# Optimization experiments

Hardware: AMD Instinct MI355X
Metric: run time of the kernel (lower is better)

The kernel has to match this reference:

```python
import jax, jax.numpy as jnp
import numpy as np

B, P, L = 256, 16, 4
NUM_ENTITY, NUM_NODE = 500000, 512
E, C1, C2 = 128, 512, 256


def setup_inputs() -> dict:
    key = jax.random.key(0)
    ks = jax.random.split(key, 13)
    inp = {
        "start_ids": jax.random.randint(ks[0], (B, P), 0, NUM_ENTITY, dtype=jnp.int32),
        "end_ids": jax.random.randint(ks[1], (B, P), 0, NUM_ENTITY, dtype=jnp.int32),
        "module_ids": jax.random.randint(ks[2], (B, P, L), 0, NUM_NODE, dtype=jnp.int32),
        "counts": jax.random.randint(ks[3], (B, P), 1, 10, dtype=jnp.int32),
        # learned parameters
        "embed": jax.random.normal(ks[4], (NUM_ENTITY, E), dtype=jnp.float32) * 0.02,
        "W": jax.random.normal(ks[5], (NUM_NODE, E, E), dtype=jnp.float32) * (1.0 / np.sqrt(E)),
        "b": jax.random.normal(ks[6], (NUM_NODE, E), dtype=jnp.float32) * 0.01,
        "W1": jax.random.normal(ks[7], (C1, 2 * E), dtype=jnp.float32) * (1.0 / np.sqrt(2 * E)),
        "b1": jnp.zeros((C1,), jnp.float32),
        "W2": jax.random.normal(ks[8], (C2, C1), dtype=jnp.float32) * (1.0 / np.sqrt(C1)),
        "b2": jnp.zeros((C2,), jnp.float32),
        "W3": jax.random.normal(ks[9], (1, C2), dtype=jnp.float32) * (1.0 / np.sqrt(C2)),
        "b3": jnp.zeros((1,), jnp.float32),
    }
    return inp


def reference(start_ids, end_ids, module_ids, counts, embed, W, b, W1, b1, W2, b2, W3, b3):
    # Embed path endpoints: [B, P, E]
    x = embed[start_ids]
    y = embed[end_ids]

    # Apply the same per-node Linear chain to both endpoint embeddings.
    # Scan over the L path steps; gather the step's weight matrices per path.
    def step(carry, mids):  # mids: [B, P]
        x, y = carry
        Wg = W[mids]            # [B, P, E, E] (out, in)
        bg = b[mids]            # [B, P, E]
        x = jnp.einsum('bpi,bpoi->bpo', x, Wg) + bg
        y = jnp.einsum('bpi,bpoi->bpo', y, Wg) + bg
        return (x, y), None

    (x, y), _ = jax.lax.scan(step, (x, y), jnp.transpose(module_ids, (2, 0, 1)))

    feat = jnp.concatenate([x, y], axis=-1)          # [B, P, 2E]
    c = counts.astype(feat.dtype)                    # path multiplicities
    pooled = jnp.einsum('bp,bpf->bf', c, feat) / jnp.sum(c, axis=1, keepdims=True)

    h = jax.nn.relu(pooled @ W1.T + b1)
    h = jax.nn.relu(h @ W2.T + b2)
    out = jax.nn.sigmoid(h @ W3.T + b3)              # [B, 1]
    return out
```

## Files before the change

kernel.cpp:

```cpp
#include <hip/hip_runtime.h>
#include <math.h>

#define BB 256
#define PP 16
#define LL 4
#define EE 128
#define NPATH (BB*PP)
#define NMOD 512
#define CC1 512
#define CC2 256

#define WS_STATE   0
#define WS_CNT     (NPATH*2*EE*4)
#define WS_OFF     (WS_CNT  + LL*NMOD*4)
#define WS_LISTS   (WS_OFF  + LL*NMOD*4)
#define WS_END     (WS_LISTS + LL*NPATH*4)

#define FMA4(A, S, Wv) do{ (A).x=fmaf((S),(Wv).x,(A).x); (A).y=fmaf((S),(Wv).y,(A).y); \
                           (A).z=fmaf((S),(Wv).z,(A).z); (A).w=fmaf((S),(Wv).w,(A).w);}while(0)

__device__ __forceinline__ unsigned short f2bf(float f) {
    unsigned u = __float_as_uint(f);
    u = (u + 0x7fffu + ((u >> 16) & 1u)) >> 16;
    return (unsigned short)u;
}
__device__ __forceinline__ float bf2f(unsigned short s) {
    return __uint_as_float(((unsigned)s) << 16);
}

__global__ __launch_bounds__(512) void k_bucket(
    const int* __restrict__ module_ids, int* __restrict__ cnt_g,
    int* __restrict__ off_g, int* __restrict__ lists)
{
    const int l = blockIdx.x, t = threadIdx.x;
    __shared__ int s[NMOD];
    __shared__ int pos[NMOD];
    s[t] = 0;
    __syncthreads();
    int mloc[8];
    #pragma unroll
    for (int j = 0; j < 8; ++j) {
        const int bp = j*512 + t;
        const int m = module_ids[bp*LL + l];
        mloc[j] = m;
        atomicAdd(&s[m], 1);
    }
    __syncthreads();
    const int c = s[t];
    for (int d = 1; d < NMOD; d <<= 1) {
        const int v = (t >= d) ? s[t-d] : 0;
        __syncthreads();
        s[t] += v;
        __syncthreads();
    }
    const int excl = s[t] - c;
    cnt_g[l*NMOD + t] = c;
    off_g[l*NMOD + t] = excl;
    pos[t] = excl;
    __syncthreads();
    #pragma unroll
    for (int j = 0; j < 8; ++j) {
        const int p = atomicAdd(&pos[mloc[j]], 1);
        lists[l*NPATH + p] = j*512 + t;
    }
}

__global__ __launch_bounds__(256) void k_seed(
    const int* __restrict__ start_ids, const int* __restrict__ end_ids,
    const float* __restrict__ embed, float* __restrict__ state)
{
    const int bp = blockIdx.x, t = threadIdx.x;
    const int id = (t < EE) ? start_ids[bp] : end_ids[bp];
    state[(size_t)bp*256 + t] = embed[(size_t)id*EE + (t & (EE-1))];
}

__global__ __launch_bounds__(256) void k_step(
    const int l, const float* __restrict__ W, const float* __restrict__ bvec,
    const int* __restrict__ cnt, const int* __restrict__ off,
    const int* __restrict__ lists, float* __restrict__ state)
{
    __shared__ unsigned short Ws[128*128];
    __shared__ float vb[32*128];
    const int m = blockIdx.x, t = threadIdx.x;
    const int n = cnt[l*NMOD + m];
    if (n == 0) return;

    {
        const int oc = t & 127, kh = t >> 7;
        const float4* Wr = (const float4*)(W + ((size_t)m*128 + oc)*128 + kh*64);
        #pragma unroll
        for (int it = 0; it < 16; ++it) {
            const float4 wv = Wr[it];
            const int k0 = kh*64 + it*4;
            Ws[(k0+0)*128 + oc] = f2bf(wv.x);
            Ws[(k0+1)*128 + oc] = f2bf(wv.y);
            Ws[(k0+2)*128 + oc] = f2bf(wv.z);
            Ws[(k0+3)*128 + oc] = f2bf(wv.w);
        }
    }

    const int* lst = lists + l*NPATH + off[l*NMOD + m];
    const int nr = 2*n;
    const int cg = t & 31;
    const int rg = t >> 5;
    const float4 bias4 = ((const float4*)(bvec + (size_t)m*128))[cg];

    for (int base = 0; base < nr; base += 32) {
        __syncthreads();
        #pragma unroll
        for (int it = 0; it < 4; ++it) {
            const int flat = it*256 + t;
            const int row = flat >> 5, c4 = flat & 31;
            float4 v = make_float4(0.f, 0.f, 0.f, 0.f);
            const int r = base + row;
            if (r < nr) {
                const int pv = lst[r >> 1]*2 + (r & 1);
                v = ((const float4*)state)[pv*32 + c4];
            }
            ((float4*)vb)[row*32 + c4] = v;
        }
        __syncthreads();

        float4 acc0 = make_float4(0,0,0,0), acc1 = make_float4(0,0,0,0);
        float4 acc2 = make_float4(0,0,0,0), acc3 = make_float4(0,0,0,0);
        const int r0 = rg*4;
        #pragma unroll 4
        for (int k0 = 0; k0 < 128; k0 += 4) {
            const ushort4 u0 = *(const ushort4*)&Ws[(k0+0)*128 + 4*cg];
            const ushort4 u1 = *(const ushort4*)&Ws[(k0+1)*128 + 4*cg];
            const ushort4 u2 = *(const ushort4*)&Ws[(k0+2)*128 + 4*cg];
            const ushort4 u3 = *(const ushort4*)&Ws[(k0+3)*128 + 4*cg];
            const int q = k0 >> 2;
            const float4 va0 = ((const float4*)vb)[(r0+0)*32 + q];
            const float4 va1 = ((const float4*)vb)[(r0+1)*32 + q];
            const float4 va2 = ((const float4*)vb)[(r0+2)*32 + q];
            const float4 va3 = ((const float4*)vb)[(r0+3)*32 + q];
            const float4 w0 = make_float4(bf2f(u0.x), bf2f(u0.y), bf2f(u0.z), bf2f(u0.w));
            const float4 w1 = make_float4(bf2f(u1.x), bf2f(u1.y), bf2f(u1.z), bf2f(u1.w));
            const float4 w2 = make_float4(bf2f(u2.x), bf2f(u2.y), bf2f(u2.z), bf2f(u2.w));
            const float4 w3 = make_float4(bf2f(u3.x), bf2f(u3.y), bf2f(u3.z), bf2f(u3.w));
            FMA4(acc0, va0.x, w0); FMA4(acc0, va0.y, w1); FMA4(acc0, va0.z, w2); FMA4(acc0, va0.w, w3);
            FMA4(acc1, va1.x, w0); FMA4(acc1, va1.y, w1); FMA4(acc1, va1.z, w2); FMA4(acc1, va1.w, w3);
            FMA4(acc2, va2.x, w0); FMA4(acc2, va2.y, w1); FMA4(acc2, va2.z, w2); FMA4(acc2, va2.w, w3);
            FMA4(acc3, va3.x, w0); FMA4(acc3, va3.y, w1); FMA4(acc3, va3.z, w2); FMA4(acc3, va3.w, w3);
        }
        float4 accs[4] = {acc0, acc1, acc2, acc3};
        #pragma unroll
        for (int i = 0; i < 4; ++i) {
            const int r = base + r0 + i;
            if (r < nr) {
                const int pv = lst[r >> 1]*2 + (r & 1);
                float4 o = make_float4(accs[i].x + bias4.x, accs[i].y + bias4.y,
                                       accs[i].z + bias4.z, accs[i].w + bias4.w);
                ((float4*)state)[pv*32 + cg] = o;
            }
        }
    }
}

__global__ __launch_bounds__(256) void k_mlp(
    const int* __restrict__ counts, const float* __restrict__ state,
    const float* __restrict__ W1, const float* __restrict__ b1,
    const float* __restrict__ W2, const float* __restrict__ b2,
    const float* __restrict__ W3, const float* __restrict__ b3,
    float* __restrict__ out)
{
    const int t = threadIdx.x;
    const int b0 = blockIdx.x * 2;
    __shared__ float pl[2][256];
    __shared__ float h1s[2][CC1];
    __shared__ float h2s[2][CC2];
    __shared__ float red[256];

    #pragma unroll
    for (int r = 0; r < 2; ++r) {
        const int b = b0 + r;
        float acc = 0.f, cs = 0.f;
        #pragma unroll
        for (int p = 0; p < PP; ++p) {
            const float cc = (float)counts[b*PP + p];
            cs += cc;
            acc = fmaf(cc, state[((size_t)(b*PP + p))*256 + t], acc);
        }
        pl[r][t] = acc / cs;
    }
    __syncthreads();

    #pragma unroll
    for (int hh = 0; hh < 2; ++hh) {
        const int col = t + hh*256;
        const float4* w4 = (const float4*)(W1 + (size_t)col*256);
        float a0 = b1[col], a1 = a0;
        for (int q = 0; q < 64; ++q) {
            const float4 wv = w4[q];
            const float4 v0 = ((const float4*)pl[0])[q];
            const float4 v1 = ((const float4*)pl[1])[q];
            a0 = fmaf(wv.x,v0.x, fmaf(wv.y,v0.y, fmaf(wv.z,v0.z, fmaf(wv.w,v0.w, a0))));
            a1 = fmaf(wv.x,v1.x, fmaf(wv.y,v1.y, fmaf(wv.z,v1.z, fmaf(wv.w,v1.w, a1))));
        }
        h1s[0][col] = fmaxf(a0, 0.f);
        h1s[1][col] = fmaxf(a1, 0.f);
    }
    __syncthreads();

    {
        const float4* w4 = (const float4*)(W2 + (size_t)t*512);
        float a0 = b2[t], a1 = a0;
        for (int q = 0; q < 128; ++q) {
            const float4 wv = w4[q];
            const float4 v0 = ((const float4*)h1s[0])[q];
            const float4 v1 = ((const float4*)h1s[1])[q];
            a0 = fmaf(wv.x,v0.x, fmaf(wv.y,v0.y, fmaf(wv.z,v0.z, fmaf(wv.w,v0.w, a0))));
            a1 = fmaf(wv.x,v1.x, fmaf(wv.y,v1.y, fmaf(wv.z,v1.z, fmaf(wv.w,v1.w, a1))));
        }
        h2s[0][t] = fmaxf(a0, 0.f);
        h2s[1][t] = fmaxf(a1, 0.f);
    }
    __syncthreads();

    {
        const int r = t >> 7, k = t & 127;
        red[t] = fmaf(W3[k], h2s[r][k], W3[k+128] * h2s[r][k+128]);
        for (int s = 64; s > 0; s >>= 1) {
            __syncthreads();
            if ((t & 127) < s) red[t] += red[t + s];
        }
        __syncthreads();
        if ((t & 127) == 0)
            out[b0 + r] = 1.f / (1.f + expf(-(red[t] + b3[0])));
    }
}

__global__ __launch_bounds__(256) void fb_path_kernel(
    const int* __restrict__ start_ids, const int* __restrict__ end_ids,
    const int* __restrict__ module_ids,
    const float* __restrict__ embed, const float* __restrict__ W,
    const float* __restrict__ bvec, float* __restrict__ feat_ws)
{
    const int bp = blockIdx.x, t = threadIdx.x;
    __shared__ float bufx[2][EE];
    __shared__ float bufy[2][EE];
    const int sid = start_ids[bp], eid = end_ids[bp];
    if (t < EE) bufx[0][t]      = embed[(size_t)sid*EE + t];
    else        bufy[0][t - EE] = embed[(size_t)eid*EE + (t - EE)];
    __syncthreads();
    const int o = t & (EE - 1);
    int cur = 0;
    for (int l = 0; l < LL; ++l) {
        const int mid = module_ids[bp*LL + l];
        const float*  vin  = (t < EE) ? bufx[cur] : bufy[cur];
        const float4* v4   = (const float4*)vin;
        const float4* wrow = (const float4*)(W + ((size_t)mid*EE + o)*EE);
        float acc = bvec[(size_t)mid*EE + o];
        #pragma unroll 8
        for (int k = 0; k < EE/4; ++k) {
            const float4 wv = wrow[k]; const float4 v = v4[k];
            acc = fmaf(wv.x,v.x, fmaf(wv.y,v.y, fmaf(wv.z,v.z, fmaf(wv.w,v.w, acc))));
        }
        if (t < EE) bufx[1-cur][o] = acc; else bufy[1-cur][o] = acc;
        __syncthreads();
        cur = 1 - cur;
    }
    feat_ws[(size_t)bp*(2*EE) + t] = (t < EE) ? bufx[cur][t] : bufy[cur][t - EE];
}

__global__ __launch_bounds__(256) void fb_mlp_kernel(
    const int* __restrict__ counts, const float* __restrict__ feat_ws,
    const float* __restrict__ W1, const float* __restrict__ b1,
    const float* __restrict__ W2, const float* __restrict__ b2,
    const float* __restrict__ W3, const float* __restrict__ b3,
    float* __restrict__ out)
{
    const int t = threadIdx.x, b0 = blockIdx.x*8;
    __shared__ float pooled[8][2*EE];
    __shared__ float h1s[8][CC1];
    __shared__ float h2s[8][CC2];
    for (int j = 0; j < 8; ++j) {
        const int b = b0 + j;
        float acc = 0.f, csum = 0.f;
        #pragma unroll
        for (int p = 0; p < PP; ++p) {
            const float cc = (float)counts[b*PP + p];
            csum += cc;
            acc = fmaf(cc, feat_ws[(size_t)(b*PP + p)*(2*EE) + t], acc);
        }
        pooled[j][t] = acc / csum;
    }
    __syncthreads();
    for (int rh = 0; rh < 2; ++rh) {
        const int r = t + rh*256;
        float acc[8]; const float bb = b1[r];
        #pragma unroll
        for (int j = 0; j < 8; ++j) acc[j] = bb;
        const float4* w4 = (const float4*)(W1 + (size_t)r*(2*EE));
        for (int k = 0; k < (2*EE)/4; ++k) {
            const float4 wv = w4[k];
            #pragma unroll
            for (int j = 0; j < 8; ++j) {
                const float4 v = ((const float4*)pooled[j])[k];
                acc[j] = fmaf(wv.x,v.x, fmaf(wv.y,v.y, fmaf(wv.z,v.z, fmaf(wv.w,v.w, acc[j]))));
            }
        }
        #pragma unroll
        for (int j = 0; j < 8; ++j) h1s[j][r] = fmaxf(acc[j], 0.f);
    }
    __syncthreads();
    {
        const int r = t;
        float acc[8]; const float bb = b2[r];
        #pragma unroll
        for (int j = 0; j < 8; ++j) acc[j] = bb;
        const float4* w4 = (const float4*)(W2 + (size_t)r*CC1);
        for (int k = 0; k < CC1/4; ++k) {
            const float4 wv = w4[k];
            #pragma unroll
            for (int j = 0; j < 8; ++j) {
                const float4 v = ((const float4*)h1s[j])[k];
                acc[j] = fmaf(wv.x,v.x, fmaf(wv.y,v.y, fmaf(wv.z,v.z, fmaf(wv.w,v.w, acc[j]))));
            }
        }
        #pragma unroll
        for (int j = 0; j < 8; ++j) h2s[j][r] = fmaxf(acc[j], 0.f);
    }
    __syncthreads();
    const int j = t >> 5, k = t & 31;
    float partial = 0.f;
    #pragma unroll
    for (int m = 0; m < CC2; m += 32)
        partial = fmaf(W3[k + m], h2s[j][k + m], partial);
    #pragma unroll
    for (int s = 16; s >= 1; s >>= 1) partial += __shfl_down(partial, s, 32);
    if (k == 0) out[b0 + j] = 1.f / (1.f + expf(-(partial + b3[0])));
}

extern "C" void kernel_launch(void* const* d_in, const int* in_sizes, int n_in,
                              void* d_out, int out_size, void* d_ws, size_t ws_size,
                              hipStream_t stream)
{
    const int*   start_ids  = (const int*)d_in[0];
    const int*   end_ids    = (const int*)d_in[1];
    const int*   module_ids = (const int*)d_in[2];
    const int*   counts     = (const int*)d_in[3];
    const float* embed      = (const float*)d_in[4];
    const float* W          = (const float*)d_in[5];
    const float* bvec       = (const float*)d_in[6];
    const float* W1         = (const float*)d_in[7];
    const float* b1         = (const float*)d_in[8];
    const float* W2         = (const float*)d_in[9];
    const float* b2         = (const float*)d_in[10];
    const float* W3         = (const float*)d_in[11];
    const float* b3         = (const float*)d_in[12];
    float* out = (float*)d_out;
    char*  ws  = (char*)d_ws;

    if (ws_size >= (size_t)WS_END) {
        float* state = (float*)(ws + WS_STATE);
        int*   cnt   = (int*)(ws + WS_CNT);
        int*   offs  = (int*)(ws + WS_OFF);
        int*   lists = (int*)(ws + WS_LISTS);

        k_bucket<<<LL, 512, 0, stream>>>(module_ids, cnt, offs, lists);
        k_seed<<<NPATH, 256, 0, stream>>>(start_ids, end_ids, embed, state);
        for (int l = 0; l < LL; ++l)
            k_step<<<NMOD, 256, 0, stream>>>(l, W, bvec, cnt, offs, lists, state);
        k_mlp<<<BB/2, 256, 0, stream>>>(counts, state, W1, b1, W2, b2, W3, b3, out);
    } else {
        float* feat_ws = (float*)d_ws;
        fb_path_kernel<<<NPATH, 256, 0, stream>>>(start_ids, end_ids, module_ids,
                                                  embed, W, bvec, feat_ws);
        fb_mlp_kernel<<<BB/8, 256, 0, stream>>>(counts, feat_ws, W1, b1, W2, b2,
                                                W3, b3, out);
    }
}
```

Baseline: 447.4 us.

## Fuse bucketing, seeding, all steps and MLP into one cooperative kernel

Replaces the seven separate launches (bucket, seed, four per-module steps, MLP) with a single cooperative kernel of 512 blocks that uses grid-wide syncs between phases. Each block loads its module's weight matrix into shared memory as bf16 once and keeps it there for all four steps, instead of reloading it every step. This removes launch gaps and repeated weight loads, at the cost of grid syncs and occupancy limits from the shared memory footprint. If the cooperative launch fails, the old multi-kernel path is used.

After: 711.5 us. 59.0% more time.

```diff
diff --git a/kernel.cpp b/kernel.cpp
--- a/kernel.cpp
+++ b/kernel.cpp
@@ -1,5 +1,8 @@
 #include <hip/hip_runtime.h>
+#include <hip/hip_cooperative_groups.h>
 #include <math.h>
+
+namespace cg = cooperative_groups;
 
 #define BB 256
 #define PP 16
@@ -26,6 +29,222 @@
 }
 __device__ __forceinline__ float bf2f(unsigned short s) {
     return __uint_as_float(((unsigned)s) << 16);
+}
+
+__global__ __launch_bounds__(256, 2) void k_fused(
+    const int* __restrict__ start_ids, const int* __restrict__ end_ids,
+    const int* __restrict__ module_ids, const int* __restrict__ counts,
+    const float* __restrict__ embed, const float* __restrict__ W,
+    const float* __restrict__ bvec,
+    const float* __restrict__ W1, const float* __restrict__ b1,
+    const float* __restrict__ W2, const float* __restrict__ b2,
+    const float* __restrict__ W3, const float* __restrict__ b3,
+    float* __restrict__ out, float* __restrict__ state,
+    int* __restrict__ cntg, int* __restrict__ offg, int* __restrict__ listsg)
+{
+    const int t   = threadIdx.x;
+    const int blk = blockIdx.x;
+    __shared__ unsigned short Ws[128*128];
+    __shared__ float vb[32*128];
+    cg::grid_group grid = cg::this_grid();
+
+    if (blk < LL) {
+        const int l = blk;
+        int* s   = (int*)vb;
+        int* pos = s + NMOD;
+        int* p   = pos + NMOD;
+        s[t] = 0; s[t + 256] = 0;
+        __syncthreads();
+        int mloc[16];
+        #pragma unroll
+        for (int j = 0; j < 16; ++j) {
+            const int bp = j*256 + t;
+            const int m = module_ids[bp*LL + l];
+            mloc[j] = m;
+            atomicAdd(&s[m], 1);
+        }
+        __syncthreads();
+        const int c0 = s[2*t], c1 = s[2*t+1];
+        const int ps = c0 + c1;
+        p[t] = ps;
+        __syncthreads();
+        for (int d = 1; d < 256; d <<= 1) {
+            const int v = (t >= d) ? p[t-d] : 0;
+            __syncthreads();
+            p[t] += v;
+            __syncthreads();
+        }
+        const int pe = p[t] - ps;
+        cntg[l*NMOD + 2*t]     = c0;
+        cntg[l*NMOD + 2*t + 1] = c1;
+        offg[l*NMOD + 2*t]     = pe;
+        offg[l*NMOD + 2*t + 1] = pe + c0;
+        pos[2*t]     = pe;
+        pos[2*t + 1] = pe + c0;
+        __syncthreads();
+        #pragma unroll
+        for (int j = 0; j < 16; ++j) {
+            const int pp = atomicAdd(&pos[mloc[j]], 1);
+            listsg[l*NPATH + pp] = j*256 + t;
+        }
+    }
+
+    {
+        const int oc = t & 127, kh = t >> 7;
+        const float4* Wr = (const float4*)(W + ((size_t)blk*128 + oc)*128 + kh*64);
+        #pragma unroll
+        for (int it = 0; it < 16; ++it) {
+            const float4 wv = Wr[it];
+            const int k0 = kh*64 + it*4;
+            Ws[(k0+0)*128 + oc] = f2bf(wv.x);
+            Ws[(k0+1)*128 + oc] = f2bf(wv.y);
+            Ws[(k0+2)*128 + oc] = f2bf(wv.z);
+            Ws[(k0+3)*128 + oc] = f2bf(wv.w);
+        }
+    }
+
+    {
+        const int g = t >> 5, c4 = t & 31;
+        #pragma unroll
+        for (int rr = 0; rr < 2; ++rr) {
+            const int row = blk*16 + g*2 + rr;
+            const int bp  = row >> 1;
+            const int id  = (row & 1) ? end_ids[bp] : start_ids[bp];
+            ((float4*)state)[(size_t)row*32 + c4] =
+                ((const float4*)(embed + (size_t)id*EE))[c4];
+        }
+    }
+
+    grid.sync();
+
+    const int cgi = t & 31;
+    const int rg  = t >> 5;
+    const float4 bias4 = ((const float4*)(bvec + (size_t)blk*EE))[cgi];
+    for (int l = 0; l < LL; ++l) {
+        const int n = cntg[l*NMOD + blk];
+        if (n > 0) {
+            const int* lst = listsg + l*NPATH + offg[l*NMOD + blk];
+            const int nr = 2*n;
+            for (int base = 0; base < nr; base += 32) {
+                __syncthreads();
+                #pragma unroll
+                for (int it = 0; it < 4; ++it) {
+                    const int flat = it*256 + t;
+                    const int row = flat >> 5, c4 = flat & 31;
+                    float4 v = make_float4(0.f, 0.f, 0.f, 0.f);
+                    const int r = base + row;
+                    if (r < nr) {
+                        const int pv = lst[r >> 1]*2 + (r & 1);
+                        v = ((const float4*)state)[(size_t)pv*32 + c4];
+                    }
+                    ((float4*)vb)[row*32 + c4] = v;
+                }
+                __syncthreads();
+
+                float4 acc0 = make_float4(0,0,0,0), acc1 = make_float4(0,0,0,0);
+                float4 acc2 = make_float4(0,0,0,0), acc3 = make_float4(0,0,0,0);
+                const int r0 = rg*4;
+                #pragma unroll 4
+                for (int k0 = 0; k0 < 128; k0 += 4) {
+                    const ushort4 u0 = *(const ushort4*)&Ws[(k0+0)*128 + 4*cgi];
+                    const ushort4 u1 = *(const ushort4*)&Ws[(k0+1)*128 + 4*cgi];
+                    const ushort4 u2 = *(const ushort4*)&Ws[(k0+2)*128 + 4*cgi];
+                    const ushort4 u3 = *(const ushort4*)&Ws[(k0+3)*128 + 4*cgi];
+                    const int q = k0 >> 2;
+                    const float4 va0 = ((const float4*)vb)[(r0+0)*32 + q];
+                    const float4 va1 = ((const float4*)vb)[(r0+1)*32 + q];
+                    const float4 va2 = ((const float4*)vb)[(r0+2)*32 + q];
+                    const float4 va3 = ((const float4*)vb)[(r0+3)*32 + q];
+                    const float4 w0 = make_float4(bf2f(u0.x), bf2f(u0.y), bf2f(u0.z), bf2f(u0.w));
+                    const float4 w1 = make_float4(bf2f(u1.x), bf2f(u1.y), bf2f(u1.z), bf2f(u1.w));
+                    const float4 w2 = make_float4(bf2f(u2.x), bf2f(u2.y), bf2f(u2.z), bf2f(u2.w));
+                    const float4 w3 = make_float4(bf2f(u3.x), bf2f(u3.y), bf2f(u3.z), bf2f(u3.w));
+                    FMA4(acc0, va0.x, w0); FMA4(acc0, va0.y, w1); FMA4(acc0, va0.z, w2); FMA4(acc0, va0.w, w3);
+                    FMA4(acc1, va1.x, w0); FMA4(acc1, va1.y, w1); FMA4(acc1, va1.z, w2); FMA4(acc1, va1.w, w3);
+                    FMA4(acc2, va2.x, w0); FMA4(acc2, va2.y, w1); FMA4(acc2, va2.z, w2); FMA4(acc2, va2.w, w3);
+                    FMA4(acc3, va3.x, w0); FMA4(acc3, va3.y, w1); FMA4(acc3, va3.z, w2); FMA4(acc3, va3.w, w3);
+                }
+                float4 accs[4] = {acc0, acc1, acc2, acc3};
+                #pragma unroll
+                for (int i = 0; i < 4; ++i) {
+                    const int r = base + r0 + i;
+                    if (r < nr) {
+                        const int pv = lst[r >> 1]*2 + (r & 1);
+                        float4 o = make_float4(accs[i].x + bias4.x, accs[i].y + bias4.y,
+                                               accs[i].z + bias4.z, accs[i].w + bias4.w);
+                        ((float4*)state)[(size_t)pv*32 + cgi] = o;
+                    }
+                }
+            }
+        }
+        grid.sync();
+    }
+
+    if (blk < BB/2) {
+        const int b0 = blk*2;
+        float* pl  = vb;
+        float* h1s = vb + 2*256;
+        float* h2s = vb + 2*256 + 2*CC1;
+        float* red = h2s + 2*CC2;
+
+        #pragma unroll
+        for (int r = 0; r < 2; ++r) {
+            const int b = b0 + r;
+            float acc = 0.f, cs = 0.f;
+            #pragma unroll
+            for (int p = 0; p < PP; ++p) {
+                const float cc = (float)counts[b*PP + p];
+                cs += cc;
+                acc = fmaf(cc, state[((size_t)(b*PP + p))*256 + t], acc);
+            }
+            pl[r*256 + t] = acc / cs;
+        }
+        __syncthreads();
+
+        #pragma unroll
+        for (int hh = 0; hh < 2; ++hh) {
+            const int col = t + hh*256;
+            const float4* w4 = (const float4*)(W1 + (size_t)col*256);
+            float a0 = b1[col], a1 = a0;
+            for (int q = 0; q < 64; ++q) {
+                const float4 wv = w4[q];
+                const float4 v0 = ((const float4*)pl)[q];
+                const float4 v1 = ((const float4*)(pl + 256))[q];
+                a0 = fmaf(wv.x,v0.x, fmaf(wv.y,v0.y, fmaf(wv.z,v0.z, fmaf(wv.w,v0.w, a0))));
+                a1 = fmaf(wv.x,v1.x, fmaf(wv.y,v1.y, fmaf(wv.z,v1.z, fmaf(wv.w,v1.w, a1))));
+            }
+            h1s[col]       = fmaxf(a0, 0.f);
+            h1s[CC1 + col] = fmaxf(a1, 0.f);
+        }
+        __syncthreads();
+
+        {
+            const float4* w4 = (const float4*)(W2 + (size_t)t*CC1);
+            float a0 = b2[t], a1 = a0;
+            for (int q = 0; q < 128; ++q) {
+                const float4 wv = w4[q];
+                const float4 v0 = ((const float4*)h1s)[q];
+                const float4 v1 = ((const float4*)(h1s + CC1))[q];
+                a0 = fmaf(wv.x,v0.x, fmaf(wv.y,v0.y, fmaf(wv.z,v0.z, fmaf(wv.w,v0.w, a0))));
+                a1 = fmaf(wv.x,v1.x, fmaf(wv.y,v1.y, fmaf(wv.z,v1.z, fmaf(wv.w,v1.w, a1))));
+            }
+            h2s[t]       = fmaxf(a0, 0.f);
+            h2s[CC2 + t] = fmaxf(a1, 0.f);
+        }
+        __syncthreads();
+
+        {
+            const int r = t >> 7, k = t & 127;
+            red[t] = fmaf(W3[k], h2s[r*CC2 + k], W3[k+128] * h2s[r*CC2 + k + 128]);
+            for (int sdx = 64; sdx > 0; sdx >>= 1) {
+                __syncthreads();
+                if ((t & 127) < sdx) red[t] += red[t + sdx];
+            }
+            __syncthreads();
+            if ((t & 127) == 0)
+                out[b0 + r] = 1.f / (1.f + expf(-(red[t] + b3[0])));
+        }
+    }
 }
 
 __global__ __launch_bounds__(512) void k_bucket(
@@ -359,6 +578,17 @@
         int*   offs  = (int*)(ws + WS_OFF);
         int*   lists = (int*)(ws + WS_LISTS);
 
+        void* args[] = {
+            (void*)&start_ids, (void*)&end_ids, (void*)&module_ids, (void*)&counts,
+            (void*)&embed, (void*)&W, (void*)&bvec,
+            (void*)&W1, (void*)&b1, (void*)&W2, (void*)&b2, (void*)&W3, (void*)&b3,
+            (void*)&out, (void*)&state, (void*)&cnt, (void*)&offs, (void*)&lists};
+
+        hipError_t e = hipLaunchCooperativeKernel(
+            reinterpret_cast<const void*>(k_fused), dim3(NMOD), dim3(256),
+            (void**)args, 0, stream);
+        if (e == hipSuccess) return;
+
         k_bucket<<<LL, 512, 0, stream>>>(module_ids, cnt, offs, lists);
         k_seed<<<NPATH, 256, 0, stream>>>(start_ids, end_ids, embed, state);
         for (int l = 0; l < LL; ++l)
```

## Replace module-bucketed step kernels with per-path fused chain over a bf16 weight copy

Applied to the files above, without the earlier changes.

Drops the bucketing kernel, the seed kernel and the four per-step kernels that grouped paths by module and reused each weight matrix from shared memory. A single chain kernel now runs all L steps for two paths per block, with each thread reading its weight row directly from global memory. A preceding pass converts all of W to bf16 so those reads move half the bytes. The trade is that weight reuse now depends on L2 rather than shared memory, and the full W (32 MB) is converted on every call.

Measured after the change: 452.4 us. About the same (+1.1%).

```diff
diff --git a/kernel.cpp b/kernel.cpp
--- a/kernel.cpp
+++ b/kernel.cpp
@@ -10,14 +10,9 @@
 #define CC1 512
 #define CC2 256
 
-#define WS_STATE   0
-#define WS_CNT     (NPATH*2*EE*4)
-#define WS_OFF     (WS_CNT  + LL*NMOD*4)
-#define WS_LISTS   (WS_OFF  + LL*NMOD*4)
-#define WS_END     (WS_LISTS + LL*NPATH*4)
-
-#define FMA4(A, S, Wv) do{ (A).x=fmaf((S),(Wv).x,(A).x); (A).y=fmaf((S),(Wv).y,(A).y); \
-                           (A).z=fmaf((S),(Wv).z,(A).z); (A).w=fmaf((S),(Wv).w,(A).w);}while(0)
+#define WS_FEAT   0
+#define WS_WBF    ((size_t)NPATH*2*EE*4)
+#define WS_BF_END (WS_WBF + (size_t)NMOD*EE*EE*2)
 
 __device__ __forceinline__ unsigned short f2bf(float f) {
     unsigned u = __float_as_uint(f);
@@ -28,134 +23,91 @@
     return __uint_as_float(((unsigned)s) << 16);
 }
 
-__global__ __launch_bounds__(512) void k_bucket(
-    const int* __restrict__ module_ids, int* __restrict__ cnt_g,
-    int* __restrict__ off_g, int* __restrict__ lists)
-{
-    const int l = blockIdx.x, t = threadIdx.x;
-    __shared__ int s[NMOD];
-    __shared__ int pos[NMOD];
-    s[t] = 0;
-    __syncthreads();
-    int mloc[8];
+__global__ __launch_bounds__(256) void k_wconv(
+    const float* __restrict__ W, unsigned short* __restrict__ Wbf)
+{
+    const size_t base = ((size_t)blockIdx.x*256 + threadIdx.x)*8;
+    const float4 a = *(const float4*)(W + base);
+    const float4 b = *(const float4*)(W + base + 4);
+    uint4 u;
+    u.x = (unsigned)f2bf(a.x) | ((unsigned)f2bf(a.y) << 16);
+    u.y = (unsigned)f2bf(a.z) | ((unsigned)f2bf(a.w) << 16);
+    u.z = (unsigned)f2bf(b.x) | ((unsigned)f2bf(b.y) << 16);
+    u.w = (unsigned)f2bf(b.z) | ((unsigned)f2bf(b.w) << 16);
+    *(uint4*)(Wbf + base) = u;
+}
+
+template<int USEBF>
+__global__ __launch_bounds__(256) void k_chain(
+    const int* __restrict__ start_ids, const int* __restrict__ end_ids,
+    const int* __restrict__ module_ids, const float* __restrict__ embed,
+    const float* __restrict__ W, const unsigned short* __restrict__ Wbf,
+    const float* __restrict__ bvec, float* __restrict__ feat)
+{
+    const int t = threadIdx.x;
+    const int p = t >> 7;
+    const int o = t & 127;
+    const int bp = blockIdx.x*2 + p;
+    __shared__ float sx[2][2][EE];
+    __shared__ float sy[2][2][EE];
+
+    sx[p][0][o] = embed[(size_t)start_ids[bp]*EE + o];
+    sy[p][0][o] = embed[(size_t)end_ids[bp]*EE + o];
+    __syncthreads();
+
+    int cur = 0;
     #pragma unroll
-    for (int j = 0; j < 8; ++j) {
-        const int bp = j*512 + t;
-        const int m = module_ids[bp*LL + l];
-        mloc[j] = m;
-        atomicAdd(&s[m], 1);
-    }
-    __syncthreads();
-    const int c = s[t];
-    for (int d = 1; d < NMOD; d <<= 1) {
-        const int v = (t >= d) ? s[t-d] : 0;
+    for (int l = 0; l < LL; ++l) {
+        const int mid = module_ids[bp*LL + l];
+        float ax = bvec[(size_t)mid*EE + o];
+        float ay = ax;
+        if (USEBF) {
+            const uint4* wr = (const uint4*)(Wbf + ((size_t)mid*EE + o)*EE);
+            #pragma unroll
+            for (int i = 0; i < EE; i += 8) {
+                const uint4 wv = wr[i >> 3];
+                const float4 xv0 = *(const float4*)&sx[p][cur][i];
+                const float4 xv1 = *(const float4*)&sx[p][cur][i+4];
+                const float4 yv0 = *(const float4*)&sy[p][cur][i];
+                const float4 yv1 = *(const float4*)&sy[p][cur][i+4];
+                const float w0 = bf2f((unsigned short)(wv.x & 0xffffu));
+                const float w1 = bf2f((unsigned short)(wv.x >> 16));
+                const float w2 = bf2f((unsigned short)(wv.y & 0xffffu));
+                const float w3 = bf2f((unsigned short)(wv.y >> 16));
+                const float w4 = bf2f((unsigned short)(wv.z & 0xffffu));
+                const float w5 = bf2f((unsigned short)(wv.z >> 16));
+                const float w6 = bf2f((unsigned short)(wv.w & 0xffffu));
+                const float w7 = bf2f((unsigned short)(wv.w >> 16));
+                ax = fmaf(w0, xv0.x, ax); ay = fmaf(w0, yv0.x, ay);
+                ax = fmaf(w1, xv0.y, ax); ay = fmaf(w1, yv0.y, ay);
+                ax = fmaf(w2, xv0.z, ax); ay = fmaf(w2, yv0.z, ay);
+                ax = fmaf(w3, xv0.w, ax); ay = fmaf(w3, yv0.w, ay);
+                ax = fmaf(w4, xv1.x, ax); ay = fmaf(w4, yv1.x, ay);
+                ax = fmaf(w5, xv1.y, ax); ay = fmaf(w5, yv1.y, ay);
+                ax = fmaf(w6, xv1.z, ax); ay = fmaf(w6, yv1.z, ay);
+                ax = fmaf(w7, xv1.w, ax); ay = fmaf(w7, yv1.w, ay);
+            }
+        } else {
+            const float4* wr = (const float4*)(W + ((size_t)mid*EE + o)*EE);
+            #pragma unroll
+            for (int i = 0; i < EE; i += 4) {
+                const float4 wv = wr[i >> 2];
+                const float4 xv = *(const float4*)&sx[p][cur][i];
+                const float4 yv = *(const float4*)&sy[p][cur][i];
+                ax = fmaf(wv.x, xv.x, ax); ay = fmaf(wv.x, yv.x, ay);
+                ax = fmaf(wv.y, xv.y, ax); ay = fmaf(wv.y, yv.y, ay);
+                ax = fmaf(wv.z, xv.z, ax); ay = fmaf(wv.z, yv.z, ay);
+                ax = fmaf(wv.w, xv.w, ax); ay = fmaf(wv.w, yv.w, ay);
+            }
+        }
+        sx[p][cur^1][o] = ax;
+        sy[p][cur^1][o] = ay;
         __syncthreads();
-        s[t] += v;
-        __syncthreads();
-    }
-    const int excl = s[t] - c;
-    cnt_g[l*NMOD + t] = c;
-    off_g[l*NMOD + t] = excl;
-    pos[t] = excl;
-    __syncthreads();
-    #pragma unroll
-    for (int j = 0; j < 8; ++j) {
-        const int p = atomicAdd(&pos[mloc[j]], 1);
-        lists[l*NPATH + p] = j*512 + t;
-    }
-}
-
-__global__ __launch_bounds__(256) void k_seed(
-    const int* __restrict__ start_ids, const int* __restrict__ end_ids,
-    const float* __restrict__ embed, float* __restrict__ state)
-{
-    const int bp = blockIdx.x, t = threadIdx.x;
-    const int id = (t < EE) ? start_ids[bp] : end_ids[bp];
-    state[(size_t)bp*256 + t] = embed[(size_t)id*EE + (t & (EE-1))];
-}
-
-__global__ __launch_bounds__(256) void k_step(
-    const int l, const float* __restrict__ W, const float* __restrict__ bvec,
-    const int* __restrict__ cnt, const int* __restrict__ off,
-    const int* __restrict__ lists, float* __restrict__ state)
-{
-    __shared__ unsigned short Ws[128*128];
-    __shared__ float vb[32*128];
-    const int m = blockIdx.x, t = threadIdx.x;
-    const int n = cnt[l*NMOD + m];
-    if (n == 0) return;
-
-    {
-        const int oc = t & 127, kh = t >> 7;
-        const float4* Wr = (const float4*)(W + ((size_t)m*128 + oc)*128 + kh*64);
-        #pragma unroll
-        for (int it = 0; it < 16; ++it) {
-            const float4 wv = Wr[it];
-            const int k0 = kh*64 + it*4;
-            Ws[(k0+0)*128 + oc] = f2bf(wv.x);
-            Ws[(k0+1)*128 + oc] = f2bf(wv.y);
-            Ws[(k0+2)*128 + oc] = f2bf(wv.z);
-            Ws[(k0+3)*128 + oc] = f2bf(wv.w);
-        }
-    }
-
-    const int* lst = lists + l*NPATH + off[l*NMOD + m];
-    const int nr = 2*n;
-    const int cg = t & 31;
-    const int rg = t >> 5;
-    const float4 bias4 = ((const float4*)(bvec + (size_t)m*128))[cg];
-
-    for (int base = 0; base < nr; base += 32) {
-        __syncthreads();
-        #pragma unroll
-        for (int it = 0; it < 4; ++it) {
-            const int flat = it*256 + t;
-            const int row = flat >> 5, c4 = flat & 31;
-            float4 v = make_float4(0.f, 0.f, 0.f, 0.f);
-            const int r = base + row;
-            if (r < nr) {
-                const int pv = lst[r >> 1]*2 + (r & 1);
-                v = ((const float4*)state)[pv*32 + c4];
-            }
-            ((float4*)vb)[row*32 + c4] = v;
-        }
-        __syncthreads();
-
-        float4 acc0 = make_float4(0,0,0,0), acc1 = make_float4(0,0,0,0);
-        float4 acc2 = make_float4(0,0,0,0), acc3 = make_float4(0,0,0,0);
-        const int r0 = rg*4;
-        #pragma unroll 4
-        for (int k0 = 0; k0 < 128; k0 += 4) {
-            const ushort4 u0 = *(const ushort4*)&Ws[(k0+0)*128 + 4*cg];
-            const ushort4 u1 = *(const ushort4*)&Ws[(k0+1)*128 + 4*cg];
-            const ushort4 u2 = *(const ushort4*)&Ws[(k0+2)*128 + 4*cg];
-            const ushort4 u3 = *(const ushort4*)&Ws[(k0+3)*128 + 4*cg];
-            const int q = k0 >> 2;
-            const float4 va0 = ((const float4*)vb)[(r0+0)*32 + q];
-            const float4 va1 = ((const float4*)vb)[(r0+1)*32 + q];
-            const float4 va2 = ((const float4*)vb)[(r0+2)*32 + q];
-            const float4 va3 = ((const float4*)vb)[(r0+3)*32 + q];
-            const float4 w0 = make_float4(bf2f(u0.x), bf2f(u0.y), bf2f(u0.z), bf2f(u0.w));
-            const float4 w1 = make_float4(bf2f(u1.x), bf2f(u1.y), bf2f(u1.z), bf2f(u1.w));
-            const float4 w2 = make_float4(bf2f(u2.x), bf2f(u2.y), bf2f(u2.z), bf2f(u2.w));
-            const float4 w3 = make_float4(bf2f(u3.x), bf2f(u3.y), bf2f(u3.z), bf2f(u3.w));
-            FMA4(acc0, va0.x, w0); FMA4(acc0, va0.y, w1); FMA4(acc0, va0.z, w2); FMA4(acc0, va0.w, w3);
-            FMA4(acc1, va1.x, w0); FMA4(acc1, va1.y, w1); FMA4(acc1, va1.z, w2); FMA4(acc1, va1.w, w3);
-            FMA4(acc2, va2.x, w0); FMA4(acc2, va2.y, w1); FMA4(acc2, va2.z, w2); FMA4(acc2, va2.w, w3);
-            FMA4(acc3, va3.x, w0); FMA4(acc3, va3.y, w1); FMA4(acc3, va3.z, w2); FMA4(acc3, va3.w, w3);
-        }
-        float4 accs[4] = {acc0, acc1, acc2, acc3};
-        #pragma unroll
-        for (int i = 0; i < 4; ++i) {
-            const int r = base + r0 + i;
-            if (r < nr) {
-                const int pv = lst[r >> 1]*2 + (r & 1);
-                float4 o = make_float4(accs[i].x + bias4.x, accs[i].y + bias4.y,
-                                       accs[i].z + bias4.z, accs[i].w + bias4.w);
-                ((float4*)state)[pv*32 + cg] = o;
-            }
-        }
-    }
+        cur ^= 1;
+    }
+
+    feat[(size_t)bp*(2*EE) + o]      = sx[p][cur][o];
+    feat[(size_t)bp*(2*EE) + EE + o] = sy[p][cur][o];
 }
 
 __global__ __launch_bounds__(256) void k_mlp(
@@ -229,108 +181,6 @@
         if ((t & 127) == 0)
             out[b0 + r] = 1.f / (1.f + expf(-(red[t] + b3[0])));
     }
-}
-
-__global__ __launch_bounds__(256) void fb_path_kernel(
-    const int* __restrict__ start_ids, const int* __restrict__ end_ids,
-    const int* __restrict__ module_ids,
-    const float* __restrict__ embed, const float* __restrict__ W,
-    const float* __restrict__ bvec, float* __restrict__ feat_ws)
-{
-    const int bp = blockIdx.x, t = threadIdx.x;
-    __shared__ float bufx[2][EE];
-    __shared__ float bufy[2][EE];
-    const int sid = start_ids[bp], eid = end_ids[bp];
-    if (t < EE) bufx[0][t]      = embed[(size_t)sid*EE + t];
-    else        bufy[0][t - EE] = embed[(size_t)eid*EE + (t - EE)];
-    __syncthreads();
-    const int o = t & (EE - 1);
-    int cur = 0;
-    for (int l = 0; l < LL; ++l) {
-        const int mid = module_ids[bp*LL + l];
-        const float*  vin  = (t < EE) ? bufx[cur] : bufy[cur];
-        const float4* v4   = (const float4*)vin;
-        const float4* wrow = (const float4*)(W + ((size_t)mid*EE + o)*EE);
-        float acc = bvec[(size_t)mid*EE + o];
-        #pragma unroll 8
-        for (int k = 0; k < EE/4; ++k) {
-            const float4 wv = wrow[k]; const float4 v = v4[k];
-            acc = fmaf(wv.x,v.x, fmaf(wv.y,v.y, fmaf(wv.z,v.z, fmaf(wv.w,v.w, acc))));
-        }
-        if (t < EE) bufx[1-cur][o] = acc; else bufy[1-cur][o] = acc;
-        __syncthreads();
-        cur = 1 - cur;
-    }
-    feat_ws[(size_t)bp*(2*EE) + t] = (t < EE) ? bufx[cur][t] : bufy[cur][t - EE];
-}
-
-__global__ __launch_bounds__(256) void fb_mlp_kernel(
-    const int* __restrict__ counts, const float* __restrict__ feat_ws,
-    const float* __restrict__ W1, const float* __restrict__ b1,
-    const float* __restrict__ W2, const float* __restrict__ b2,
-    const float* __restrict__ W3, const float* __restrict__ b3,
-    float* __restrict__ out)
-{
-    const int t = threadIdx.x, b0 = blockIdx.x*8;
-    __shared__ float pooled[8][2*EE];
-    __shared__ float h1s[8][CC1];
-    __shared__ float h2s[8][CC2];
-    for (int j = 0; j < 8; ++j) {
-        const int b = b0 + j;
-        float acc = 0.f, csum = 0.f;
-        #pragma unroll
-        for (int p = 0; p < PP; ++p) {
-            const float cc = (float)counts[b*PP + p];
-            csum += cc;
-            acc = fmaf(cc, feat_ws[(size_t)(b*PP + p)*(2*EE) + t], acc);
-        }
-        pooled[j][t] = acc / csum;
-    }
-    __syncthreads();
-    for (int rh = 0; rh < 2; ++rh) {
-        const int r = t + rh*256;
-        float acc[8]; const float bb = b1[r];
-        #pragma unroll
-        for (int j = 0; j < 8; ++j) acc[j] = bb;
-        const float4* w4 = (const float4*)(W1 + (size_t)r*(2*EE));
-        for (int k = 0; k < (2*EE)/4; ++k) {
-            const float4 wv = w4[k];
-            #pragma unroll
-            for (int j = 0; j < 8; ++j) {
-                const float4 v = ((const float4*)pooled[j])[k];
-                acc[j] = fmaf(wv.x,v.x, fmaf(wv.y,v.y, fmaf(wv.z,v.z, fmaf(wv.w,v.w, acc[j]))));
-            }
-        }
-        #pragma unroll
-        for (int j = 0; j < 8; ++j) h1s[j][r] = fmaxf(acc[j], 0.f);
-    }
-    __syncthreads();
-    {
-        const int r = t;
-        float acc[8]; const float bb = b2[r];
-        #pragma unroll
-        for (int j = 0; j < 8; ++j) acc[j] = bb;
-        const float4* w4 = (const float4*)(W2 + (size_t)r*CC1);
-        for (int k = 0; k < CC1/4; ++k) {
-            const float4 wv = w4[k];
-            #pragma unroll
-            for (int j = 0; j < 8; ++j) {
-                const float4 v = ((const float4*)h1s[j])[k];
-                acc[j] = fmaf(wv.x,v.x, fmaf(wv.y,v.y, fmaf(wv.z,v.z, fmaf(wv.w,v.w, acc[j]))));
-            }
-        }
-        #pragma unroll
-        for (int j = 0; j < 8; ++j) h2s[j][r] = fmaxf(acc[j], 0.f);
-    }
-    __syncthreads();
-    const int j = t >> 5, k = t & 31;
-    float partial = 0.f;
-    #pragma unroll
-    for (int m = 0; m < CC2; m += 32)
-        partial = fmaf(W3[k + m], h2s[j][k + m], partial);
-    #pragma unroll
-    for (int s = 16; s >= 1; s >>= 1) partial += __shfl_down(partial, s, 32);
-    if (k == 0) out[b0 + j] = 1.f / (1.f + expf(-(partial + b3[0])));
 }
 
 extern "C" void kernel_launch(void* const* d_in, const int* in_sizes, int n_in,
@@ -350,25 +200,19 @@
     const float* b2         = (const float*)d_in[10];
     const float* W3         = (const float*)d_in[11];
     const float* b3         = (const float*)d_in[12];
-    float* out = (float*)d_out;
-    char*  ws  = (char*)d_ws;
-
-    if (ws_size >= (size_t)WS_END) {
-        float* state = (float*)(ws + WS_STATE);
-        int*   cnt   = (int*)(ws + WS_CNT);
-        int*   offs  = (int*)(ws + WS_OFF);
-        int*   lists = (int*)(ws + WS_LISTS);
-
-        k_bucket<<<LL, 512, 0, stream>>>(module_ids, cnt, offs, lists);
-        k_seed<<<NPATH, 256, 0, stream>>>(start_ids, end_ids, embed, state);
-        for (int l = 0; l < LL; ++l)
-            k_step<<<NMOD, 256, 0, stream>>>(l, W, bvec, cnt, offs, lists, state);
-        k_mlp<<<BB/2, 256, 0, stream>>>(counts, state, W1, b1, W2, b2, W3, b3, out);
+    float* out  = (float*)d_out;
+    char*  ws   = (char*)d_ws;
+    float* feat = (float*)(ws + WS_FEAT);
+
+    if (ws_size >= WS_BF_END) {
+        unsigned short* Wbf = (unsigned short*)(ws + WS_WBF);
+        k_wconv<<<4096, 256, 0, stream>>>(W, Wbf);
+        k_chain<1><<<NPATH/2, 256, 0, stream>>>(start_ids, end_ids, module_ids,
+                                                embed, W, Wbf, bvec, feat);
     } else {
-        float* feat_ws = (float*)d_ws;
-        fb_path_kernel<<<NPATH, 256, 0, stream>>>(start_ids, end_ids, module_ids,
-                                                  embed, W, bvec, feat_ws);
-        fb_mlp_kernel<<<BB/8, 256, 0, stream>>>(counts, feat_ws, W1, b1, W2, b2,
-                                                W3, b3, out);
-    }
-}
+        k_chain<0><<<NPATH/2, 256, 0, stream>>>(start_ids, end_ids, module_ids,
+                                                embed, W, (const unsigned short*)0,
+                                                bvec, feat);
+    }
+    k_mlp<<<BB/2, 256, 0, stream>>>(counts, feat, W1, b1, W2, b2, W3, b3, out);
+}
```
